# Kernel tuning notes

Hardware: AMD Instinct MI355X
Metric: run time of the kernel (lower is better)

The kernel has to match this reference:

```python
import jax, jax.numpy as jnp
import numpy as np

B, S, D, H = 8, 1024, 1024, 16
DH = D // H
LN_EPS = 1e-5
SLOPE = 0.01  # nn.LeakyReLU default negative_slope


def _ln(x, g, b):
    m = x.mean(-1, keepdims=True)
    v = ((x - m) ** 2).mean(-1, keepdims=True)
    return (x - m) / jnp.sqrt(v + LN_EPS) * g + b


def _leaky(x):
    return jnp.where(x >= 0, x, SLOPE * x)


def setup_inputs() -> dict:
    key = jax.random.key(0)
    ks = jax.random.split(key, 6)
    q = jax.random.normal(ks[0], (B, S, D), dtype=jnp.float32)
    masks = jnp.ones((B, S), dtype=jnp.int32)  # all-valid mask (masked_fill is a no-op)
    w1 = jax.random.normal(ks[1], (D, D), dtype=jnp.float32) * 0.02
    b1 = jnp.zeros((D,), jnp.float32)
    w2 = jax.random.normal(ks[2], (D, D), dtype=jnp.float32) * 0.02
    b2 = jnp.zeros((D,), jnp.float32)
    ones = jnp.ones((D,), jnp.float32)
    zeros = jnp.zeros((D,), jnp.float32)
    return dict(q=q, masks=masks,
                w1=w1, b1=b1, ln1_g=ones, ln1_b=zeros,
                w2=w2, b2=b2, ln2_g=ones, ln2_b=zeros,
                anf_g=ones, anf_b=zeros,
                an1_g=ones, an1_b=zeros,
                an2_g=ones, an2_b=zeros)


def reference(q, masks, w1, b1, ln1_g, ln1_b, w2, b2, ln2_g, ln2_b,
              anf_g, anf_b, an1_g, an1_b, an2_g, an2_b):
    # --- multi-head cosine-similarity attention (k = v = q, no projections) ---
    qh = q.reshape(B, S, H, DH).transpose(0, 2, 1, 3)  # (B,H,S,DH) == separate_heads
    qn = qh / jnp.clip(jnp.linalg.norm(qh, axis=-1, keepdims=True), 1e-8)
    # cosine similarity scores, softmax over keys
    w = jax.nn.softmax(jnp.einsum('bhqd,bhkd->bhqk', qn, qn), axis=-1)
    # masked_fill AFTER softmax (faithful to source: mask per (batch, query))
    w = jnp.where(masks[:, None, :, None] == 0, jnp.float32(-1e9), w)
    heads = jnp.einsum('bhqk,bhkd->bhqd', w, qh)
    attn = heads.transpose(0, 2, 1, 3).reshape(B, S, D)  # concat_heads
    # --- add_norm1 (dropout=0.5 but eval mode => identity) ---
    y1 = _ln(q + attn, an1_g, an1_b)
    # --- PositionWiseFFN: Linear->LN->LeakyReLU x2, then internal AddNorm ---
    h = _leaky(_ln(y1 @ w1 + b1, ln1_g, ln1_b))
    y = _leaky(_ln(h @ w2 + b2, ln2_g, ln2_b))
    y2 = _ln(y1 + y, anf_g, anf_b)
    # --- add_norm2 ---
    return _ln(y1 + y2, an2_g, an2_b)
```

## Files before the change

kernel.cpp:

```cpp
#include <hip/hip_runtime.h>
#include <hip/hip_bf16.h>

#define BB 8
#define SS 1024
#define DD 1024
#define HH 16

typedef __attribute__((ext_vector_type(8))) short short8;
typedef __attribute__((ext_vector_type(8))) __bf16 bf16x8;
typedef __attribute__((ext_vector_type(4))) float f32x4;

__device__ inline float bf2f(unsigned short h){
  unsigned u = ((unsigned)h) << 16;
  return __builtin_bit_cast(float, u);
}
__device__ inline unsigned short f2bf(float f){
  unsigned u = __builtin_bit_cast(unsigned, f);
  u += 0x7fffu + ((u >> 16) & 1u);
  return (unsigned short)(u >> 16);
}
__device__ inline f32x4 mfma16(short8 a, short8 b, f32x4 c){
  return __builtin_amdgcn_mfma_f32_16x16x32_bf16(
      __builtin_bit_cast(bf16x8, a), __builtin_bit_cast(bf16x8, b), c, 0, 0, 0);
}
__device__ inline void gld_lds16(const unsigned short* g, unsigned short* l){
  __builtin_amdgcn_global_load_lds((const __attribute__((address_space(1))) void*)g,
      (__attribute__((address_space(3))) void*)l, 16, 0, 0);
}

__global__ __launch_bounds__(256) void prep_w(const float* __restrict__ w1,
                                              const float* __restrict__ w2,
                                              unsigned short* __restrict__ w1T,
                                              unsigned short* __restrict__ w2T){
  __shared__ float tile[64][65];
  const float* src = blockIdx.z ? w2 : w1;
  unsigned short* dst = blockIdx.z ? w2T : w1T;
  int k0 = blockIdx.x * 64, n0 = blockIdx.y * 64;
  int tx = threadIdx.x & 63, ty = threadIdx.x >> 6;
#pragma unroll
  for (int r = 0; r < 16; ++r)
    tile[ty + 4*r][tx] = src[(k0 + ty + 4*r) * DD + n0 + tx];
  __syncthreads();
#pragma unroll
  for (int r = 0; r < 16; ++r)
    dst[(n0 + ty + 4*r) * DD + k0 + tx] = f2bf(tile[tx][ty + 4*r]);
}

__global__ __launch_bounds__(256) void prep_q(const float* __restrict__ q,
                                              unsigned short* __restrict__ kf,
                                              unsigned short* __restrict__ vf,
                                              unsigned short* __restrict__ qb){
  __shared__ float tile[64][65];
  __shared__ float rinv[64];
  int bh = blockIdx.x >> 4, st = blockIdx.x & 15;
  int b = bh >> 4, h = bh & 15;
  int t = threadIdx.x;
  int tx = t & 63, ty = t >> 6;
  int srow = b * SS + st * 64;
#pragma unroll
  for (int r = 0; r < 16; ++r)
    tile[ty + 4*r][tx] = q[(size_t)(srow + ty + 4*r) * DD + h * 64 + tx];
  __syncthreads();
  {
    int s = t >> 2, p = t & 3;
    float ssum = 0.f;
#pragma unroll
    for (int i = 0; i < 16; ++i){ float v = tile[s][p*16 + i]; ssum += v * v; }
    ssum += __shfl_xor(ssum, 1);
    ssum += __shfl_xor(ssum, 2);
    if (p == 0) rinv[s] = 1.0f / fmaxf(sqrtf(ssum), 1e-8f);
  }
  __syncthreads();
#pragma unroll
  for (int r = 0; r < 16; ++r)
    qb[(size_t)(srow + ty + 4*r) * DD + h * 64 + tx] = f2bf(tile[ty + 4*r][tx]);
#pragma unroll
  for (int v = 0; v < 2; ++v){
    int idx = t * 2 + v;
    int c_l = idx >> 6, lane = idx & 63;
    int g2 = c_l >> 2, c = (c_l >> 1) & 1, hf = c_l & 1;
    int lrq = lane & 15, lgq = lane >> 4;
    int s = g2 * 32 + (lrq >> 2) * 8 + c * 4 + (lrq & 3);
    int d0 = hf * 32 + lgq * 8;
    float rv = rinv[s];
    short8 o;
#pragma unroll
    for (int e = 0; e < 8; ++e) o[e] = (short)f2bf(tile[s][d0 + e] * rv);
    *(short8*)(kf + ((size_t)(bh * 128 + st * 8 + c_l) * 64 + lane) * 8) = o;
  }
#pragma unroll
  for (int v = 0; v < 2; ++v){
    int idx = t * 2 + v;
    int kt2 = idx >> 8, db = (idx >> 6) & 3, lane = idx & 63;
    int d = db * 16 + (lane & 15);
    int k0 = kt2 * 32 + (lane >> 4) * 8;
    short8 o;
#pragma unroll
    for (int e = 0; e < 8; ++e) o[e] = (short)f2bf(tile[k0 + e][d]);
    *(short8*)(vf + ((size_t)((bh * 32 + st * 2 + kt2) * 4 + db) * 512 + lane * 8)) = o;
  }
}

#define NPH 16
__global__ __launch_bounds__(512, 4) void attn_kern(const unsigned short* __restrict__ kf,
                                                    const unsigned short* __restrict__ vf,
                                                    const int* __restrict__ masks,
                                                    unsigned short* __restrict__ attnb){
  __shared__ unsigned short Kb[3][8][512];
  __shared__ unsigned short Vb[3][8][512];
  __shared__ int anym;
  const int bh = blockIdx.x, b = bh >> 4, h = bh & 15;
  const int by = blockIdx.y;
  const int t = threadIdx.x, w = t >> 6, l = t & 63;
  const int lr = l & 15, lg = l >> 4;
  if (t == 0) anym = 0;
  __syncthreads();
  if (t < 256 && masks[b * SS + by * 256 + t] == 0) anym = 1;

  short8 aQ[2][2];
#pragma unroll
  for (int c = 0; c < 2; ++c)
#pragma unroll
    for (int hf = 0; hf < 2; ++hf)
      aQ[c][hf] = *(const short8*)(kf +
          ((size_t)(bh * 128 + (by * 8 + w) * 4 + c * 2 + hf) * 64 + l) * 8);

#define STAGE(ph, bf) do {                                                            \
    if (w < 4){                                                                       \
      gld_lds16(kf + ((size_t)(bh * 128 + (2*(ph)) * 4 + w) * 64 + l) * 8,            \
                &Kb[bf][w][0]);                                                       \
      gld_lds16(kf + ((size_t)(bh * 128 + (2*(ph)+1) * 4 + w) * 64 + l) * 8,          \
                &Kb[bf][4 + w][0]);                                                   \
    } else {                                                                          \
      gld_lds16(vf + ((size_t)((bh * 32 + 2*(ph)) * 4 + (w - 4)) * 512 + l * 8),      \
                &Vb[bf][w - 4][0]);                                                   \
      gld_lds16(vf + ((size_t)((bh * 32 + 2*(ph)+1) * 4 + (w - 4)) * 512 + l * 8),    \
                &Vb[bf][4 + (w - 4)][0]);                                             \
    }                                                                                 \
  } while (0)

  STAGE(0, 0);
  STAGE(1, 1);
  asm volatile("s_waitcnt vmcnt(2) lgkmcnt(0)" ::: "memory");
  __builtin_amdgcn_s_barrier();

  f32x4 o[2][4] = {};
  float rsum[2] = {0.f, 0.f};

  for (int ph = 0; ph < NPH; ++ph){
    const int cur = ph % 3;
    if (ph + 2 < NPH) STAGE(ph + 2, (ph + 2) % 3);
#pragma unroll
    for (int gi = 0; gi < 2; ++gi){
      short8 bK[2][2];
#pragma unroll
      for (int c = 0; c < 2; ++c)
#pragma unroll
        for (int hf = 0; hf < 2; ++hf)
          bK[c][hf] = *(const short8*)&Kb[cur][gi * 4 + c * 2 + hf][l * 8];
      f32x4 sc[2][2];
#pragma unroll
      for (int qc = 0; qc < 2; ++qc)
#pragma unroll
        for (int c = 0; c < 2; ++c){
          f32x4 z = {0.f, 0.f, 0.f, 0.f};
          z = mfma16(bK[c][0], aQ[qc][0], z);
          z = mfma16(bK[c][1], aQ[qc][1], z);
          sc[qc][c] = z;
        }
      bf16x8 pav[2];
#pragma unroll
      for (int qc = 0; qc < 2; ++qc)
#pragma unroll
        for (int c = 0; c < 2; ++c)
#pragma unroll
          for (int j = 0; j < 4; ++j){
            float pv = __expf(sc[qc][c][j] - 1.0f);
            rsum[qc] += pv;
            pav[qc][c * 4 + j] = (__bf16)pv;
          }
      short8 pa0 = __builtin_bit_cast(short8, pav[0]);
      short8 pa1 = __builtin_bit_cast(short8, pav[1]);
#pragma unroll
      for (int db = 0; db < 4; ++db){
        short8 bV = *(const short8*)&Vb[cur][gi * 4 + db][l * 8];
        o[0][db] = mfma16(pa0, bV, o[0][db]);
        o[1][db] = mfma16(pa1, bV, o[1][db]);
      }
    }
    if (ph + 1 < NPH){
      asm volatile("s_waitcnt lgkmcnt(0)" ::: "memory");
      if (ph + 2 < NPH) asm volatile("s_waitcnt vmcnt(2)" ::: "memory");
      else              asm volatile("s_waitcnt vmcnt(0)" ::: "memory");
      __builtin_amdgcn_s_barrier();
    }
  }

  float invq[2];
#pragma unroll
  for (int qc = 0; qc < 2; ++qc){
    float r = rsum[qc];
    r += __shfl_xor(r, 16);
    r += __shfl_xor(r, 32);
    invq[qc] = 1.0f / r;
  }
#pragma unroll
  for (int qc = 0; qc < 2; ++qc){
    float invj[4];
#pragma unroll
    for (int j = 0; j < 4; ++j) invj[j] = __shfl(invq[qc], lg * 4 + j);
#pragma unroll
    for (int db = 0; db < 4; ++db)
#pragma unroll
      for (int j = 0; j < 4; ++j){
        int qrow = by * 256 + w * 32 + lg * 8 + qc * 4 + j;
        float val = o[qc][db][j] * invj[j];
        if (anym && masks[b * SS + qrow] == 0){
          float vs = 0.f;
          for (int kt = 0; kt < 32; ++kt)
            for (int lgp = 0; lgp < 4; ++lgp){
              const unsigned short* vp = vf +
                  ((size_t)((bh * 32 + kt) * 4 + db) * 512 + (lgp * 16 + lr) * 8);
              for (int e = 0; e < 8; ++e) vs += bf2f(vp[e]);
            }
          val = -1e9f * vs;
        }
        attnb[(size_t)(b * SS + qrow) * DD + h * 64 + db * 16 + lr] = f2bf(val);
      }
  }
#undef STAGE
}

__device__ inline float2 block_reduce2(float a, float bq){
  __shared__ float sm[8];
#pragma unroll
  for (int off = 1; off < 64; off <<= 1){
    a += __shfl_xor(a, off);
    bq += __shfl_xor(bq, off);
  }
  int w = threadIdx.x >> 6;
  if ((threadIdx.x & 63) == 0){ sm[2*w] = a; sm[2*w + 1] = bq; }
  __syncthreads();
  float2 r;
  r.x = sm[0] + sm[2] + sm[4] + sm[6];
  r.y = sm[1] + sm[3] + sm[5] + sm[7];
  __syncthreads();
  return r;
}

__global__ __launch_bounds__(256) void addnorm1(const unsigned short* __restrict__ qb,
                                                const unsigned short* __restrict__ attnb,
                                                const float* __restrict__ g,
                                                const float* __restrict__ bt,
                                                unsigned short* __restrict__ y1b){
  int row = blockIdx.x, t = threadIdx.x;
  ushort4 qv = *(const ushort4*)(qb + (size_t)row * DD + t * 4);
  ushort4 av = *(const ushort4*)(attnb + (size_t)row * DD + t * 4);
  float x[4] = { bf2f(qv.x) + bf2f(av.x), bf2f(qv.y) + bf2f(av.y),
                 bf2f(qv.z) + bf2f(av.z), bf2f(qv.w) + bf2f(av.w) };
  float s = 0.f, ssq = 0.f;
#pragma unroll
  for (int i = 0; i < 4; ++i){ s += x[i]; ssq += x[i] * x[i]; }
  float2 r = block_reduce2(s, ssq);
  float m = r.x * (1.0f / DD);
  float rs = rsqrtf(r.y * (1.0f / DD) - m * m + 1e-5f);
  float4 gv = *(const float4*)(g + t * 4);
  float4 bv = *(const float4*)(bt + t * 4);
  float y[4] = { (x[0]-m)*rs*gv.x + bv.x, (x[1]-m)*rs*gv.y + bv.y,
                 (x[2]-m)*rs*gv.z + bv.z, (x[3]-m)*rs*gv.w + bv.w };
  ushort4 ob = { f2bf(y[0]), f2bf(y[1]), f2bf(y[2]), f2bf(y[3]) };
  *(ushort4*)(y1b + (size_t)row * DD + t * 4) = ob;
}

__global__ __launch_bounds__(256, 2) void gemm_bias(const unsigned short* __restrict__ X,
                                                    const unsigned short* __restrict__ WT,
                                                    const float* __restrict__ bias,
                                                    unsigned short* __restrict__ out){
  __shared__ unsigned short As[3][128 * 32];
  __shared__ unsigned short Bs[3][128 * 32];
  int t = threadIdx.x, l = t & 63, w = t >> 6;
  int wm = w >> 1, wn = w & 1;
  int lr = l & 15, lg = l >> 4;
  int bm = blockIdx.x * 128, bn = blockIdx.y * 128;
  f32x4 acc[4][4] = {};
  int r = t >> 2, cb = (t & 3) * 8;

#define GSTAGE(kt, bf) do {                                                        \
    gld_lds16(X  + (size_t)(bm +      r) * 1024 + (kt) * 32 + cb,                  \
              &As[bf][w * 512]);                                                   \
    gld_lds16(X  + (size_t)(bm + 64 + r) * 1024 + (kt) * 32 + cb,                  \
              &As[bf][2048 + w * 512]);                                            \
    gld_lds16(WT + (size_t)(bn +      r) * 1024 + (kt) * 32 + cb,                  \
              &Bs[bf][w * 512]);                                                   \
    gld_lds16(WT + (size_t)(bn + 64 + r) * 1024 + (kt) * 32 + cb,                  \
              &Bs[bf][2048 + w * 512]);                                            \
  } while (0)

  GSTAGE(0, 0);
  GSTAGE(1, 1);
  asm volatile("s_waitcnt vmcnt(4)" ::: "memory");
  __builtin_amdgcn_s_barrier();

  for (int kt = 0; kt < 32; ++kt){
    const int cur = kt % 3;
    if (kt + 2 < 32) GSTAGE(kt + 2, (kt + 2) % 3);
    short8 aA[4], bB[4];
#pragma unroll
    for (int i = 0; i < 4; ++i)
      aA[i] = *(const short8*)&As[cur][(wm * 64 + i * 16 + lr) * 32 + lg * 8];
#pragma unroll
    for (int i = 0; i < 4; ++i)
      bB[i] = *(const short8*)&Bs[cur][(wn * 64 + i * 16 + lr) * 32 + lg * 8];
#pragma unroll
    for (int mi = 0; mi < 4; ++mi)
#pragma unroll
      for (int ni = 0; ni < 4; ++ni)
        acc[mi][ni] = mfma16(aA[mi], bB[ni], acc[mi][ni]);
    if (kt + 1 < 32){
      asm volatile("s_waitcnt lgkmcnt(0)" ::: "memory");
      if (kt + 2 < 32) asm volatile("s_waitcnt vmcnt(4)" ::: "memory");
      else             asm volatile("s_waitcnt vmcnt(0)" ::: "memory");
      __builtin_amdgcn_s_barrier();
    }
  }
#undef GSTAGE
#pragma unroll
  for (int ni = 0; ni < 4; ++ni){
    int col = bn + wn * 64 + ni * 16 + lr;
    float bv = bias[col];
#pragma unroll
    for (int mi = 0; mi < 4; ++mi){
      int row0 = bm + wm * 64 + mi * 16 + lg * 4;
#pragma unroll
      for (int j = 0; j < 4; ++j)
        out[(size_t)(row0 + j) * 1024 + col] = f2bf(acc[mi][ni][j] + bv);
    }
  }
}

__global__ __launch_bounds__(256) void ln_leaky(const unsigned short* __restrict__ in,
                                                const float* __restrict__ g,
                                                const float* __restrict__ bt,
                                                unsigned short* __restrict__ out){
  int row = blockIdx.x, t = threadIdx.x;
  ushort4 iv = *(const ushort4*)(in + (size_t)row * DD + t * 4);
  float x[4] = { bf2f(iv.x), bf2f(iv.y), bf2f(iv.z), bf2f(iv.w) };
  float s = 0.f, ssq = 0.f;
#pragma unroll
  for (int i = 0; i < 4; ++i){ s += x[i]; ssq += x[i] * x[i]; }
  float2 r = block_reduce2(s, ssq);
  float m = r.x * (1.0f / DD);
  float rs = rsqrtf(r.y * (1.0f / DD) - m * m + 1e-5f);
  float4 gv = *(const float4*)(g + t * 4);
  float4 bv = *(const float4*)(bt + t * 4);
  ushort4 ov;
  {
    float v0 = (x[0]-m)*rs*gv.x + bv.x; v0 = v0 >= 0.f ? v0 : 0.01f*v0; ov.x = f2bf(v0);
    float v1 = (x[1]-m)*rs*gv.y + bv.y; v1 = v1 >= 0.f ? v1 : 0.01f*v1; ov.y = f2bf(v1);
    float v2 = (x[2]-m)*rs*gv.z + bv.z; v2 = v2 >= 0.f ? v2 : 0.01f*v2; ov.z = f2bf(v2);
    float v3 = (x[3]-m)*rs*gv.w + bv.w; v3 = v3 >= 0.f ? v3 : 0.01f*v3; ov.w = f2bf(v3);
  }
  *(ushort4*)(out + (size_t)row * DD + t * 4) = ov;
}

__global__ __launch_bounds__(256) void final_kern(const unsigned short* __restrict__ g2,
                                                  const unsigned short* __restrict__ y1,
                                                  const float* __restrict__ ln2g, const float* __restrict__ ln2b,
                                                  const float* __restrict__ anfg, const float* __restrict__ anfb,
                                                  const float* __restrict__ an2g, const float* __restrict__ an2b,
                                                  float* __restrict__ out){
  int row = blockIdx.x, t = threadIdx.x;
  ushort4 iv = *(const ushort4*)(g2 + (size_t)row * DD + t * 4);
  ushort4 y1v = *(const ushort4*)(y1 + (size_t)row * DD + t * 4);
  float x[4] = { bf2f(iv.x), bf2f(iv.y), bf2f(iv.z), bf2f(iv.w) };
  float yy1[4] = { bf2f(y1v.x), bf2f(y1v.y), bf2f(y1v.z), bf2f(y1v.w) };
  float s = 0.f, ssq = 0.f;
#pragma unroll
  for (int i = 0; i < 4; ++i){ s += x[i]; ssq += x[i]*x[i]; }
  float2 r = block_reduce2(s, ssq);
  float m = r.x * (1.0f / DD);
  float rs = rsqrtf(r.y * (1.0f / DD) - m*m + 1e-5f);
  float4 gv = *(const float4*)(ln2g + t * 4);
  float4 bv = *(const float4*)(ln2b + t * 4);
  float y[4] = { (x[0]-m)*rs*gv.x + bv.x, (x[1]-m)*rs*gv.y + bv.y,
                 (x[2]-m)*rs*gv.z + bv.z, (x[3]-m)*rs*gv.w + bv.w };
#pragma unroll
  for (int i = 0; i < 4; ++i) y[i] = y[i] >= 0.f ? y[i] : 0.01f*y[i];

  float tv[4]; s = 0.f; ssq = 0.f;
#pragma unroll
  for (int i = 0; i < 4; ++i){ tv[i] = yy1[i] + y[i]; s += tv[i]; ssq += tv[i]*tv[i]; }
  r = block_reduce2(s, ssq);
  m = r.x * (1.0f / DD);
  rs = rsqrtf(r.y * (1.0f / DD) - m*m + 1e-5f);
  gv = *(const float4*)(anfg + t * 4);
  bv = *(const float4*)(anfb + t * 4);
  float y2[4] = { (tv[0]-m)*rs*gv.x + bv.x, (tv[1]-m)*rs*gv.y + bv.y,
                  (tv[2]-m)*rs*gv.z + bv.z, (tv[3]-m)*rs*gv.w + bv.w };

  float u[4]; s = 0.f; ssq = 0.f;
#pragma unroll
  for (int i = 0; i < 4; ++i){ u[i] = yy1[i] + y2[i]; s += u[i]; ssq += u[i]*u[i]; }
  r = block_reduce2(s, ssq);
  m = r.x * (1.0f / DD);
  rs = rsqrtf(r.y * (1.0f / DD) - m*m + 1e-5f);
  gv = *(const float4*)(an2g + t * 4);
  bv = *(const float4*)(an2b + t * 4);
  float4 ov = { (u[0]-m)*rs*gv.x + bv.x, (u[1]-m)*rs*gv.y + bv.y,
                (u[2]-m)*rs*gv.z + bv.z, (u[3]-m)*rs*gv.w + bv.w };
  *(float4*)(out + (size_t)row * DD + t * 4) = ov;
}

extern "C" void kernel_launch(void* const* d_in, const int* in_sizes, int n_in,
                              void* d_out, int out_size, void* d_ws, size_t ws_size,
                              hipStream_t stream){
  const float* q    = (const float*)d_in[0];
  const int* masks  = (const int*)d_in[1];
  const float* w1   = (const float*)d_in[2];
  const float* b1   = (const float*)d_in[3];
  const float* ln1g = (const float*)d_in[4];
  const float* ln1b = (const float*)d_in[5];
  const float* w2   = (const float*)d_in[6];
  const float* b2   = (const float*)d_in[7];
  const float* ln2g = (const float*)d_in[8];
  const float* ln2b = (const float*)d_in[9];
  const float* anfg = (const float*)d_in[10];
  const float* anfb = (const float*)d_in[11];
  const float* an1g = (const float*)d_in[12];
  const float* an1b = (const float*)d_in[13];
  const float* an2g = (const float*)d_in[14];
  const float* an2b = (const float*)d_in[15];

  char* ws = (char*)d_ws;
  unsigned short* w1T  = (unsigned short*)(ws + 0);
  unsigned short* w2T  = (unsigned short*)(ws + 2097152);
  unsigned short* kf   = (unsigned short*)(ws + 4194304);
  unsigned short* vf   = (unsigned short*)(ws + 20971520);
  unsigned short* attn = (unsigned short*)(ws + 37748736);
  unsigned short* y1b  = (unsigned short*)(ws + 54525952);
  unsigned short* qb   = (unsigned short*)(ws + 71303168);
  unsigned short* g1   = kf;
  unsigned short* hbuf = vf;
  unsigned short* g2   = attn;
  float* outp = (float*)d_out;

  prep_w<<<dim3(16, 16, 2), 256, 0, stream>>>(w1, w2, w1T, w2T);
  prep_q<<<dim3(2048), 256, 0, stream>>>(q, kf, vf, qb);
  attn_kern<<<dim3(128, 4), 512, 0, stream>>>(kf, vf, masks, attn);
  addnorm1<<<dim3(8192), 256, 0, stream>>>(qb, attn, an1g, an1b, y1b);
  gemm_bias<<<dim3(64, 8), 256, 0, stream>>>(y1b, w1T, b1, g1);
  ln_leaky<<<dim3(8192), 256, 0, stream>>>(g1, ln1g, ln1b, hbuf);
  gemm_bias<<<dim3(64, 8), 256, 0, stream>>>(hbuf, w2T, b2, g2);
  final_kern<<<dim3(8192), 256, 0, stream>>>(g2, y1b, ln2g, ln2b, anfg, anfb, an2g, an2b, outp);
}
```

Before: 158.1 us.

## Use native exp2 with prescaled keys, MFMA row sums, and remapped GEMM block order

```diff
diff --git a/kernel.cpp b/kernel.cpp
--- a/kernel.cpp
+++ b/kernel.cpp
@@ -82,7 +82,7 @@
     int lrq = lane & 15, lgq = lane >> 4;
     int s = g2 * 32 + (lrq >> 2) * 8 + c * 4 + (lrq & 3);
     int d0 = hf * 32 + lgq * 8;
-    float rv = rinv[s];
+    float rv = rinv[s] * 1.20112240878645f;
     short8 o;
 #pragma unroll
     for (int e = 0; e < 8; ++e) o[e] = (short)f2bf(tile[s][d0 + e] * rv);
@@ -125,6 +125,9 @@
       aQ[c][hf] = *(const short8*)(kf +
           ((size_t)(bh * 128 + (by * 8 + w) * 4 + c * 2 + hf) * 64 + l) * 8);
 
+  const short ONEB = (short)0x3F80;
+  const short8 ones = {ONEB, ONEB, ONEB, ONEB, ONEB, ONEB, ONEB, ONEB};
+
 #define STAGE(ph, bf) do {                                                            \
     if (w < 4){                                                                       \
       gld_lds16(kf + ((size_t)(bh * 128 + (2*(ph)) * 4 + w) * 64 + l) * 8,            \
@@ -145,7 +148,7 @@
   __builtin_amdgcn_s_barrier();
 
   f32x4 o[2][4] = {};
-  float rsum[2] = {0.f, 0.f};
+  f32x4 rsacc[2] = {};
 
   for (int ph = 0; ph < NPH; ++ph){
     const int cur = ph % 3;
@@ -175,12 +178,14 @@
         for (int c = 0; c < 2; ++c)
 #pragma unroll
           for (int j = 0; j < 4; ++j){
-            float pv = __expf(sc[qc][c][j] - 1.0f);
-            rsum[qc] += pv;
+            float x = sc[qc][c][j], pv;
+            asm("v_exp_f32 %0, %1" : "=v"(pv) : "v"(x));
             pav[qc][c * 4 + j] = (__bf16)pv;
           }
       short8 pa0 = __builtin_bit_cast(short8, pav[0]);
       short8 pa1 = __builtin_bit_cast(short8, pav[1]);
+      rsacc[0] = mfma16(pa0, ones, rsacc[0]);
+      rsacc[1] = mfma16(pa1, ones, rsacc[1]);
 #pragma unroll
       for (int db = 0; db < 4; ++db){
         short8 bV = *(const short8*)&Vb[cur][gi * 4 + db][l * 8];
@@ -196,19 +201,11 @@
     }
   }
 
-  float invq[2];
-#pragma unroll
-  for (int qc = 0; qc < 2; ++qc){
-    float r = rsum[qc];
-    r += __shfl_xor(r, 16);
-    r += __shfl_xor(r, 32);
-    invq[qc] = 1.0f / r;
-  }
 #pragma unroll
   for (int qc = 0; qc < 2; ++qc){
     float invj[4];
 #pragma unroll
-    for (int j = 0; j < 4; ++j) invj[j] = __shfl(invq[qc], lg * 4 + j);
+    for (int j = 0; j < 4; ++j) invj[j] = 1.0f / rsacc[qc][j];
 #pragma unroll
     for (int db = 0; db < 4; ++db)
 #pragma unroll
@@ -281,7 +278,9 @@
   int t = threadIdx.x, l = t & 63, w = t >> 6;
   int wm = w >> 1, wn = w & 1;
   int lr = l & 15, lg = l >> 4;
-  int bm = blockIdx.x * 128, bn = blockIdx.y * 128;
+  int id = blockIdx.x;
+  int bm = (((id & 7) << 3) + ((id >> 3) & 7)) * 128;
+  int bn = (id >> 6) * 128;
   f32x4 acc[4][4] = {};
   int r = t >> 2, cb = (t & 3) * 8;
 
@@ -448,8 +447,8 @@
   prep_q<<<dim3(2048), 256, 0, stream>>>(q, kf, vf, qb);
   attn_kern<<<dim3(128, 4), 512, 0, stream>>>(kf, vf, masks, attn);
   addnorm1<<<dim3(8192), 256, 0, stream>>>(qb, attn, an1g, an1b, y1b);
-  gemm_bias<<<dim3(64, 8), 256, 0, stream>>>(y1b, w1T, b1, g1);
+  gemm_bias<<<dim3(512), 256, 0, stream>>>(y1b, w1T, b1, g1);
   ln_leaky<<<dim3(8192), 256, 0, stream>>>(g1, ln1g, ln1b, hbuf);
-  gemm_bias<<<dim3(64, 8), 256, 0, stream>>>(hbuf, w2T, b2, g2);
+  gemm_bias<<<dim3(512), 256, 0, stream>>>(hbuf, w2T, b2, g2);
   final_kern<<<dim3(8192), 256, 0, stream>>>(g2, y1b, ln2g, ln2b, anfg, anfb, an2g, an2b, outp);
 }
```

Result: faster. 155.0 us (-2.0%).
